# Performance work log

Measured on AMD Instinct MI355X. Metric: run time of the kernel, lower is better.

## Reference

```python
import jax, jax.numpy as jnp
import numpy as np

EPS = 1e-13

def masked_softmax(x, mask):
    # Non-memory-efficient path of the original: softmax(x*mask), re-mask, renormalize.
    p = jax.nn.softmax(x * mask, axis=-1) * mask
    return p / (jnp.sum(p, axis=-1, keepdims=True) + EPS)

def setup_inputs() -> dict:
    key = jax.random.key(0)
    ka, kb, kma, kmb = jax.random.split(key, 4)
    B, La, Lb, D = 32, 1024, 1024, 256
    a = jax.random.normal(ka, (B, La, D), dtype=jnp.float32)
    b = jax.random.normal(kb, (B, Lb, D), dtype=jnp.float32)
    mask_a = jax.random.randint(kma, (B, La, 1), 0, 2, dtype=jnp.int32)
    mask_b = jax.random.randint(kmb, (B, Lb, 1), 0, 2, dtype=jnp.int32)
    return {"a": a, "b": b, "mask_a": mask_a, "mask_b": mask_b}

def reference(a, b, mask_a, mask_b):
    # a: [B, La, D], b: [B, Lb, D], mask_a: [B, La, 1], mask_b: [B, Lb, 1]
    ma = mask_a.astype(a.dtype)  # [B, La, 1]
    mb = mask_b.astype(b.dtype)  # [B, Lb, 1]
    attn = jnp.einsum('bid,bjd->bij', a, b)            # [B, La, Lb]
    amask = ma * jnp.swapaxes(mb, 1, 2)                 # outer product mask [B, La, Lb]
    weight_for_a = masked_softmax(attn, amask)          # softmax over Lb
    attended_a = jnp.einsum('bij,bjd->bid', weight_for_a, b)  # [B, La, D]
    attn_t = jnp.swapaxes(attn, 1, 2)                   # [B, Lb, La]
    amask_t = jnp.swapaxes(amask, 1, 2)
    weight_for_b = masked_softmax(attn_t, amask_t)      # softmax over La
    attended_b = jnp.einsum('bji,bid->bjd', weight_for_b, a)  # [B, Lb, D]
    return (attended_a, attended_b)
```

## Files before the change

### kernel.cpp

```cpp
#include <hip/hip_runtime.h>
#include <math.h>
#include <stdint.h>


#define NB    32
#define SEQ   1024
#define DIM   256
#define BM    128
#define BN    64
#define SHIFT 60.0f
#define PS    1048

typedef unsigned int uint;
typedef unsigned short ushort;
typedef __attribute__((ext_vector_type(8)))  short short8;
typedef __attribute__((ext_vector_type(16))) float f32x16;

#define HL_BATCH  (64 * 1024 * 8)
#define HL_TENSOR ((size_t)NB * HL_BATCH)
#define T_BATCH   (128 * 256 * 8)
#define T_TENSOR  ((size_t)NB * T_BATCH)
#define WS_NEED   ((2 * HL_TENSOR + 2 * T_TENSOR) * sizeof(ushort))

__device__ __forceinline__ ushort bf16_rn(float x) {
    union { float f; uint u; } v; v.f = x;
    uint r = v.u + 0x7fffu + ((v.u >> 16) & 1u);
    return (ushort)(r >> 16);
}
__device__ __forceinline__ float bf16_to_f(ushort h) {
    union { uint u; float f; } v; v.u = ((uint)h) << 16;
    return v.f;
}
__device__ __forceinline__ void gl_lds16(const ushort* g, ushort* l) {
    __builtin_amdgcn_global_load_lds(
        (const __attribute__((address_space(1))) void*)g,
        (__attribute__((address_space(3))) void*)l, 16, 0, 0);
}

#define TSTR 264
__global__ __launch_bounds__(256)
void prepass(const float* __restrict__ A, const float* __restrict__ Bt,
             ushort* __restrict__ aHL, ushort* __restrict__ bHL,
             ushort* __restrict__ aT,  ushort* __restrict__ bT)
{
    const int tensor = blockIdx.z;
    const float* src = tensor ? Bt : A;
    ushort* hl = tensor ? bHL : aHL;
    ushort* tp = tensor ? bT  : aT;
    const int batch = blockIdx.y;
    const int tid   = threadIdx.x;

    __shared__ float tile[8 * TSTR];

    ushort* hlb = hl + (size_t)batch * HL_BATCH;

    for (int it = 0; it < 8; ++it) {
        const int soct = blockIdx.x * 8 + it;
        const int s0   = soct * 8;
        if (it) __syncthreads();

        {
            const int oct = tid >> 3, srow = tid & 7;
            const float* rp = src + ((size_t)batch * SEQ + s0 + srow) * DIM + oct * 8;
            float4 x0 = *(const float4*)rp;
            float4 x1 = *(const float4*)(rp + 4);
            float xs[8] = {x0.x, x0.y, x0.z, x0.w, x1.x, x1.y, x1.z, x1.w};
            short8 hv, lv;
            #pragma unroll
            for (int j = 0; j < 8; ++j) {
                ushort h = bf16_rn(xs[j]);
                hv[j] = (short)h;
                lv[j] = (short)bf16_rn(xs[j] - bf16_to_f(h));
            }
            *(short8*)(hlb + (size_t)oct * 8192 + (size_t)(s0 + srow) * 8)        = hv;
            *(short8*)(hlb + (size_t)(oct + 32) * 8192 + (size_t)(s0 + srow) * 8) = lv;
        }

        const float* sb = src + ((size_t)batch * SEQ + s0) * DIM;
        #pragma unroll
        for (int i = 0; i < 2; ++i) {
            int idx = tid + i * 256;
            int r = idx >> 6, c = idx & 63;
            float4 v = *((const float4*)(sb + (size_t)r * DIM) + c);
            *(float4*)&tile[r * TSTR + c * 4] = v;
        }
        __syncthreads();
        {
            ushort* tpb = tp + (size_t)batch * T_BATCH + (size_t)soct * 2048;
            int d = tid;
            short8 hv;
            #pragma unroll
            for (int j = 0; j < 8; ++j)
                hv[j] = (short)bf16_rn(tile[j * TSTR + d]);
            *(short8*)(tpb + (size_t)d * 8) = hv;
        }
    }
}

__global__ __launch_bounds__(512, 2)
void attend3(const ushort* __restrict__ aHL, const ushort* __restrict__ bHL,
             const ushort* __restrict__ aT,  const ushort* __restrict__ bT,
             const int*    __restrict__ ma,  const int*    __restrict__ mb,
             float*        __restrict__ out)
{
    __shared__ __align__(16) ushort Ks2[64 * 512];
    __shared__ __align__(16) ushort Vt2[8 * 2048];
    __shared__ __align__(16) ushort Ph[8 * PS];
    __shared__ float msk[SEQ];
    __shared__ float lpart[2][BM];
    __shared__ float invs[BM];

    const int bx   = blockIdx.x;
    const int xcd  = bx & 7;
    const int slot = bx >> 3;
    const int rb   = slot & 7;
    const int pg   = slot >> 3;
    const int pair = xcd + 8 * pg;
    const int batch = pair >> 1;
    const int dir   = pair & 1;
    const int row0  = rb * BM;

    const ushort* hlX = dir ? bHL : aHL;
    const ushort* hlY = dir ? aHL : bHL;
    const ushort* tY  = dir ? aT  : bT;
    const int*    mx  = dir ? mb  : ma;
    const int*    my  = dir ? ma  : mb;
    float* o = out + (size_t)dir * NB * SEQ * DIM;

    const int tid  = threadIdx.x;
    const int lane = tid & 63;
    const int wave = tid >> 6;
    const int l31  = lane & 31;
    const int lh   = lane >> 5;
    const int rw   = wave >> 1;
    const int cw   = wave & 1;

    const ushort* hlXb = hlX + (size_t)batch * HL_BATCH;
    const ushort* hlYb = hlY + (size_t)batch * HL_BATCH;
    const ushort* tYb  = tY  + (size_t)batch * T_BATCH;

    const ushort* ksrc = hlYb + (size_t)(wave * 8) * 8192 + (size_t)lane * 8;
    ushort*       kdst = Ks2 + wave * 8 * 512 + lane * 8;
    const ushort* vsrc = tYb + (size_t)wave * 2048 + (size_t)lane * 8;
    ushort*       vdst = Vt2 + wave * 2048 + lane * 8;

    #pragma unroll
    for (int i = 0; i < 8; ++i) gl_lds16(ksrc + (size_t)i * 8192, kdst + i * 512);
    #pragma unroll
    for (int i = 0; i < 4; ++i) gl_lds16(vsrc + i * 512, vdst + i * 512);

    for (int i = tid; i < SEQ; i += 512) msk[i] = (float)my[batch * SEQ + i];

    const int qrow = row0 + rw * 32 + l31;
    short8 qhi[16], qlo[16];
    {
        const ushort* qb = hlXb + (size_t)lh * 8192 + (size_t)qrow * 8;
        #pragma unroll
        for (int kk = 0; kk < 16; ++kk) {
            qhi[kk] = *(const short8*)(qb + (size_t)(2 * kk) * 8192);
            qlo[kk] = *(const short8*)(qb + (size_t)(2 * kk + 32) * 8192);
        }
    }

    f32x16 oacc[4];
    #pragma unroll
    for (int t = 0; t < 4; ++t)
        #pragma unroll
        for (int r = 0; r < 16; ++r) oacc[t][r] = 0.f;
    float lsum[16];
    #pragma unroll
    for (int r = 0; r < 16; ++r) lsum[r] = 0.f;

    __syncthreads();

    for (int nt = 0; nt < SEQ / BN; ++nt) {
        const int key0 = nt * BN;
        const float mkv = msk[key0 + cw * 32 + l31];

        f32x16 a1, a2;
        #pragma unroll
        for (int r = 0; r < 16; ++r) { a1[r] = 0.f; a2[r] = 0.f; }
        const int kcol = (cw * 32 + l31) * 8;
        #pragma unroll
        for (int kk = 0; kk < 16; ++kk) {
            short8 bhi = *(const short8*)&Ks2[(2 * kk + lh) * 512 + kcol];
            a1 = __builtin_amdgcn_mfma_f32_32x32x16_bf16(qhi[kk], bhi, a1, 0, 0, 0);
            a2 = __builtin_amdgcn_mfma_f32_32x32x16_bf16(qlo[kk], bhi, a2, 0, 0, 0);
        }
        #pragma unroll
        for (int kk = 0; kk < 16; ++kk) {
            short8 blo = *(const short8*)&Ks2[(2 * kk + lh + 32) * 512 + kcol];
            a2 = __builtin_amdgcn_mfma_f32_32x32x16_bf16(qhi[kk], blo, a2, 0, 0, 0);
        }

        const int key  = cw * 32 + l31;
        const int koct = key >> 3, kj = key & 7;
        #pragma unroll
        for (int r = 0; r < 16; ++r) {
            float s = a1[r] + a2[r];
            float p = __expf(s - SHIFT) * mkv;
            lsum[r] += p;
            int qr = rw * 32 + (r & 3) + ((r >> 2) << 3) + (lh << 2);
            Ph[koct * PS + qr * 8 + kj] = bf16_rn(p);
        }
        __syncthreads();

        if (nt + 1 < SEQ / BN) {
            const ushort* ks = ksrc + (size_t)(key0 + BN) * 8;
            #pragma unroll
            for (int i = 0; i < 8; ++i) gl_lds16(ks + (size_t)i * 8192, kdst + i * 512);
        }

        const int prow = (rw * 32 + l31) * 8;
        #pragma unroll
        for (int kb = 0; kb < 4; ++kb) {
            short8 pa = *(const short8*)&Ph[(2 * kb + lh) * PS + prow];
            #pragma unroll
            for (int t = 0; t < 4; ++t) {
                int dim = cw * 128 + t * 32 + l31;
                short8 vf = *(const short8*)&Vt2[(2 * kb + lh) * 2048 + dim * 8];
                oacc[t] = __builtin_amdgcn_mfma_f32_32x32x16_bf16(pa, vf, oacc[t], 0, 0, 0);
            }
        }
        __syncthreads();

        if (nt + 1 < SEQ / BN) {
            const ushort* vs = vsrc + ((size_t)(key0 + BN) >> 3) * 2048;
            #pragma unroll
            for (int i = 0; i < 4; ++i) gl_lds16(vs + i * 512, vdst + i * 512);
        }
    }

    #pragma unroll
    for (int r = 0; r < 16; ++r) {
        float v = lsum[r];
        v += __shfl_xor(v, 1, 64);
        v += __shfl_xor(v, 2, 64);
        v += __shfl_xor(v, 4, 64);
        v += __shfl_xor(v, 8, 64);
        v += __shfl_xor(v, 16, 64);
        if (l31 == 0) {
            int row = rw * 32 + (r & 3) + ((r >> 2) << 3) + (lh << 2);
            lpart[cw][row] = v;
        }
    }
    __syncthreads();
    if (tid < BM) {
        float l = lpart[0][tid] + lpart[1][tid];
        int valid = mx[batch * SEQ + row0 + tid];
        invs[tid] = (valid != 0 && l > 0.f) ? 1.f / l : 0.f;
    }
    __syncthreads();

    float* ob = o + ((size_t)batch * SEQ + row0) * DIM;
    #pragma unroll
    for (int r = 0; r < 16; ++r) {
        int rloc = rw * 32 + (r & 3) + ((r >> 2) << 3) + (lh << 2);
        float inv = invs[rloc];
        #pragma unroll
        for (int t = 0; t < 4; ++t) {
            int d = cw * 128 + t * 32 + l31;
            ob[(size_t)rloc * DIM + d] = oacc[t][r] * inv;
        }
    }
}

#define F_KS_STR 520
#define F_P_STR  136
#define F_BM 64
#define F_BN 64
__global__ __launch_bounds__(256, 1)
void attend_mfma(const float* __restrict__ X, const float* __restrict__ Y,
                 const int* __restrict__ mx, const int* __restrict__ my,
                 float* __restrict__ out)
{
    __shared__ ushort Ks[F_BN * F_KS_STR];
    __shared__ ushort Ps[F_BM * F_P_STR];
    __shared__ float  mk[F_BN];
    __shared__ float  lpart[2][F_BM];
    __shared__ float  invs[F_BM];

    const int tid = threadIdx.x, lane = tid & 63, wave = tid >> 6;
    const int l31 = lane & 31, lh = lane >> 5;
    const int rw = wave >> 1, cw = wave & 1;
    const int batch = blockIdx.y, row0 = blockIdx.x * F_BM;
    const float* Xb = X + (size_t)batch * SEQ * DIM;
    const float* Yb = Y + (size_t)batch * SEQ * DIM;

    float4 kreg[16]; int mreg = 0;
    #pragma unroll
    for (int i = 0; i < 16; ++i) {
        int idx = tid + (i << 8); int r = idx >> 6, c4 = idx & 63;
        kreg[i] = *((const float4*)(Yb + (size_t)r * DIM) + c4);
    }
    if (tid < F_BN) mreg = my[batch * SEQ + tid];

    short8 qhi[16], qlo[16];
    {
        const float* qrow = Xb + (size_t)(row0 + rw * 32 + l31) * DIM + lh * 8;
        #pragma unroll
        for (int kk = 0; kk < 16; ++kk) {
            const float* p = qrow + kk * 16;
            float4 x0 = *(const float4*)p; float4 x1 = *(const float4*)(p + 4);
            float xs[8] = {x0.x, x0.y, x0.z, x0.w, x1.x, x1.y, x1.z, x1.w};
            #pragma unroll
            for (int j = 0; j < 8; ++j) {
                ushort h = bf16_rn(xs[j]);
                qhi[kk][j] = (short)h;
                qlo[kk][j] = (short)bf16_rn(xs[j] - bf16_to_f(h));
            }
        }
    }
    f32x16 oacc[4];
    #pragma unroll
    for (int t = 0; t < 4; ++t)
        #pragma unroll
        for (int r = 0; r < 16; ++r) oacc[t][r] = 0.f;
    float lsum[16];
    #pragma unroll
    for (int r = 0; r < 16; ++r) lsum[r] = 0.f;

    for (int nt = 0; nt < SEQ / F_BN; ++nt) {
        if (nt) __syncthreads();
        #pragma unroll
        for (int i = 0; i < 16; ++i) {
            int idx = tid + (i << 8); int r = idx >> 6, c4 = idx & 63;
            float f[4] = {kreg[i].x, kreg[i].y, kreg[i].z, kreg[i].w};
            ushort hh[4], ll[4];
            #pragma unroll
            for (int q = 0; q < 4; ++q) { hh[q] = bf16_rn(f[q]); ll[q] = bf16_rn(f[q] - bf16_to_f(hh[q])); }
            ushort4 hv; hv.x=hh[0];hv.y=hh[1];hv.z=hh[2];hv.w=hh[3];
            ushort4 lv; lv.x=ll[0];lv.y=ll[1];lv.z=ll[2];lv.w=ll[3];
            *(ushort4*)&Ks[r * F_KS_STR + c4 * 4] = hv;
            *(ushort4*)&Ks[r * F_KS_STR + 256 + c4 * 4] = lv;
        }
        if (tid < F_BN) mk[tid] = (float)mreg;
        __syncthreads();
        if (nt + 1 < SEQ / F_BN) {
            const float* Ybn = Yb + (size_t)(nt + 1) * F_BN * DIM;
            #pragma unroll
            for (int i = 0; i < 16; ++i) {
                int idx = tid + (i << 8); int r = idx >> 6, c4 = idx & 63;
                kreg[i] = *((const float4*)(Ybn + (size_t)r * DIM) + c4);
            }
            if (tid < F_BN) mreg = my[batch * SEQ + (nt + 1) * F_BN + tid];
        }
        f32x16 a1, a2, a3;
        #pragma unroll
        for (int r = 0; r < 16; ++r) { a1[r]=0.f; a2[r]=0.f; a3[r]=0.f; }
        const int krow = (cw * 32 + l31) * F_KS_STR;
        #pragma unroll
        for (int kk = 0; kk < 16; ++kk) {
            int col = kk * 16 + lh * 8;
            short8 bhi = *(const short8*)&Ks[krow + col];
            short8 blo = *(const short8*)&Ks[krow + 256 + col];
            a1 = __builtin_amdgcn_mfma_f32_32x32x16_bf16(qhi[kk], bhi, a1, 0, 0, 0);
            a2 = __builtin_amdgcn_mfma_f32_32x32x16_bf16(qlo[kk], bhi, a2, 0, 0, 0);
            a3 = __builtin_amdgcn_mfma_f32_32x32x16_bf16(qhi[kk], blo, a3, 0, 0, 0);
        }
        const float mkv = mk[cw * 32 + l31];
        #pragma unroll
        for (int r = 0; r < 16; ++r) {
            float s = a1[r] + a2[r] + a3[r];
            float p = __expf(s - SHIFT) * mkv;
            lsum[r] += p;
            ushort ph = bf16_rn(p);
            ushort pl = bf16_rn(p - bf16_to_f(ph));
            int prow = rw * 32 + (r & 3) + ((r >> 2) << 3) + (lh << 2);
            int pcol = cw * 32 + l31;
            Ps[prow * F_P_STR + pcol] = ph;
            Ps[prow * F_P_STR + 64 + pcol] = pl;
        }
        __syncthreads();
        const int prow = (rw * 32 + l31) * F_P_STR;
        #pragma unroll
        for (int kb = 0; kb < 4; ++kb) {
            int pcol = kb * 16 + lh * 8;
            short8 pa_hi = *(const short8*)&Ps[prow + pcol];
            short8 pa_lo = *(const short8*)&Ps[prow + 64 + pcol];
            #pragma unroll
            for (int t = 0; t < 4; ++t) {
                int d0 = cw * 128 + t * 32 + l31;
                short8 vf;
                #pragma unroll
                for (int j = 0; j < 8; ++j) vf[j] = (short)Ks[(pcol + j) * F_KS_STR + d0];
                oacc[t] = __builtin_amdgcn_mfma_f32_32x32x16_bf16(pa_hi, vf, oacc[t], 0, 0, 0);
                oacc[t] = __builtin_amdgcn_mfma_f32_32x32x16_bf16(pa_lo, vf, oacc[t], 0, 0, 0);
            }
        }
    }
    #pragma unroll
    for (int r = 0; r < 16; ++r) {
        float v = lsum[r];
        v += __shfl_xor(v, 1, 64); v += __shfl_xor(v, 2, 64); v += __shfl_xor(v, 4, 64);
        v += __shfl_xor(v, 8, 64); v += __shfl_xor(v, 16, 64);
        if (l31 == 0) {
            int row = rw * 32 + (r & 3) + ((r >> 2) << 3) + (lh << 2);
            lpart[cw][row] = v;
        }
    }
    __syncthreads();
    if (tid < F_BM) {
        float l = lpart[0][tid] + lpart[1][tid];
        int valid = mx[batch * SEQ + row0 + tid];
        invs[tid] = (valid != 0 && l > 0.f) ? 1.f / l : 0.f;
    }
    __syncthreads();
    float* ob = out + ((size_t)batch * SEQ + row0) * DIM;
    #pragma unroll
    for (int r = 0; r < 16; ++r) {
        int rloc = rw * 32 + (r & 3) + ((r >> 2) << 3) + (lh << 2);
        float inv = invs[rloc];
        #pragma unroll
        for (int t = 0; t < 4; ++t) {
            int d = cw * 128 + t * 32 + l31;
            ob[(size_t)rloc * DIM + d] = oacc[t][r] * inv;
        }
    }
}

extern "C" void kernel_launch(void* const* d_in, const int* in_sizes, int n_in,
                              void* d_out, int out_size, void* d_ws, size_t ws_size,
                              hipStream_t stream) {
    const float* a  = (const float*)d_in[0];
    const float* b  = (const float*)d_in[1];
    const int*   ma = (const int*)d_in[2];
    const int*   mb = (const int*)d_in[3];
    float* out = (float*)d_out;

    if (ws_size >= WS_NEED) {
        ushort* wsu = (ushort*)d_ws;
        ushort* aHL = wsu;
        ushort* bHL = wsu + HL_TENSOR;
        ushort* aT  = wsu + 2 * HL_TENSOR;
        ushort* bT  = wsu + 2 * HL_TENSOR + T_TENSOR;

        prepass<<<dim3(SEQ / 64, NB, 2), 256, 0, stream>>>(a, b, aHL, bHL, aT, bT);
        attend3<<<dim3(512, 1, 1), 512, 0, stream>>>(aHL, bHL, aT, bT, ma, mb, out);
    } else {
        float* out_a = out;
        float* out_b = out + (size_t)NB * SEQ * DIM;
        dim3 grid(SEQ / F_BM, NB), block(256);
        attend_mfma<<<grid, block, 0, stream>>>(a, b, ma, mb, out_a);
        attend_mfma<<<grid, block, 0, stream>>>(b, a, mb, ma, out_b);
    }
}
```

Baseline: 317.2 us.

## Read V fragments directly from global, split accumulators, raise MFMA priority, widen prepass grid

The attention kernel stops staging V tiles into LDS and reads the transposed bf16 V fragments straight from global memory inside the PV MFMA loop. This drops the Vt2 buffer and its async copies and frees LDS. The QK cross-term now uses a third accumulator to break the dependency chain on a2, and s_setprio brackets the MFMA loops. The prepass is flattened to one 8-row octet per block with an 8x larger grid. The direct global V reads may expose latency that the LDS staging used to hide.

```diff
diff --git a/kernel.cpp b/kernel.cpp
--- a/kernel.cpp
+++ b/kernel.cpp
@@ -54,46 +54,43 @@
 
     ushort* hlb = hl + (size_t)batch * HL_BATCH;
 
-    for (int it = 0; it < 8; ++it) {
-        const int soct = blockIdx.x * 8 + it;
-        const int s0   = soct * 8;
-        if (it) __syncthreads();
-
-        {
-            const int oct = tid >> 3, srow = tid & 7;
-            const float* rp = src + ((size_t)batch * SEQ + s0 + srow) * DIM + oct * 8;
-            float4 x0 = *(const float4*)rp;
-            float4 x1 = *(const float4*)(rp + 4);
-            float xs[8] = {x0.x, x0.y, x0.z, x0.w, x1.x, x1.y, x1.z, x1.w};
-            short8 hv, lv;
-            #pragma unroll
-            for (int j = 0; j < 8; ++j) {
-                ushort h = bf16_rn(xs[j]);
-                hv[j] = (short)h;
-                lv[j] = (short)bf16_rn(xs[j] - bf16_to_f(h));
-            }
-            *(short8*)(hlb + (size_t)oct * 8192 + (size_t)(s0 + srow) * 8)        = hv;
-            *(short8*)(hlb + (size_t)(oct + 32) * 8192 + (size_t)(s0 + srow) * 8) = lv;
-        }
-
-        const float* sb = src + ((size_t)batch * SEQ + s0) * DIM;
-        #pragma unroll
-        for (int i = 0; i < 2; ++i) {
-            int idx = tid + i * 256;
-            int r = idx >> 6, c = idx & 63;
-            float4 v = *((const float4*)(sb + (size_t)r * DIM) + c);
-            *(float4*)&tile[r * TSTR + c * 4] = v;
-        }
-        __syncthreads();
-        {
-            ushort* tpb = tp + (size_t)batch * T_BATCH + (size_t)soct * 2048;
-            int d = tid;
-            short8 hv;
-            #pragma unroll
-            for (int j = 0; j < 8; ++j)
-                hv[j] = (short)bf16_rn(tile[j * TSTR + d]);
-            *(short8*)(tpb + (size_t)d * 8) = hv;
-        }
+    const int soct = blockIdx.x;
+    const int s0   = soct * 8;
+
+    {
+        const int oct = tid >> 3, srow = tid & 7;
+        const float* rp = src + ((size_t)batch * SEQ + s0 + srow) * DIM + oct * 8;
+        float4 x0 = *(const float4*)rp;
+        float4 x1 = *(const float4*)(rp + 4);
+        float xs[8] = {x0.x, x0.y, x0.z, x0.w, x1.x, x1.y, x1.z, x1.w};
+        short8 hv, lv;
+        #pragma unroll
+        for (int j = 0; j < 8; ++j) {
+            ushort h = bf16_rn(xs[j]);
+            hv[j] = (short)h;
+            lv[j] = (short)bf16_rn(xs[j] - bf16_to_f(h));
+        }
+        *(short8*)(hlb + (size_t)oct * 8192 + (size_t)(s0 + srow) * 8)        = hv;
+        *(short8*)(hlb + (size_t)(oct + 32) * 8192 + (size_t)(s0 + srow) * 8) = lv;
+    }
+
+    const float* sb = src + ((size_t)batch * SEQ + s0) * DIM;
+    #pragma unroll
+    for (int i = 0; i < 2; ++i) {
+        int idx = tid + i * 256;
+        int r = idx >> 6, c = idx & 63;
+        float4 v = *((const float4*)(sb + (size_t)r * DIM) + c);
+        *(float4*)&tile[r * TSTR + c * 4] = v;
+    }
+    __syncthreads();
+    {
+        ushort* tpb = tp + (size_t)batch * T_BATCH + (size_t)soct * 2048;
+        int d = tid;
+        short8 hv;
+        #pragma unroll
+        for (int j = 0; j < 8; ++j)
+            hv[j] = (short)bf16_rn(tile[j * TSTR + d]);
+        *(short8*)(tpb + (size_t)d * 8) = hv;
     }
 }
 
@@ -104,7 +101,6 @@
              float*        __restrict__ out)
 {
     __shared__ __align__(16) ushort Ks2[64 * 512];
-    __shared__ __align__(16) ushort Vt2[8 * 2048];
     __shared__ __align__(16) ushort Ph[8 * PS];
     __shared__ float msk[SEQ];
     __shared__ float lpart[2][BM];
@@ -141,13 +137,9 @@
 
     const ushort* ksrc = hlYb + (size_t)(wave * 8) * 8192 + (size_t)lane * 8;
     ushort*       kdst = Ks2 + wave * 8 * 512 + lane * 8;
-    const ushort* vsrc = tYb + (size_t)wave * 2048 + (size_t)lane * 8;
-    ushort*       vdst = Vt2 + wave * 2048 + lane * 8;
 
     #pragma unroll
     for (int i = 0; i < 8; ++i) gl_lds16(ksrc + (size_t)i * 8192, kdst + i * 512);
-    #pragma unroll
-    for (int i = 0; i < 4; ++i) gl_lds16(vsrc + i * 512, vdst + i * 512);
 
     for (int i = tid; i < SEQ; i += 512) msk[i] = (float)my[batch * SEQ + i];
 
@@ -177,10 +169,11 @@
         const int key0 = nt * BN;
         const float mkv = msk[key0 + cw * 32 + l31];
 
-        f32x16 a1, a2;
-        #pragma unroll
-        for (int r = 0; r < 16; ++r) { a1[r] = 0.f; a2[r] = 0.f; }
+        f32x16 a1, a2, a3;
+        #pragma unroll
+        for (int r = 0; r < 16; ++r) { a1[r] = 0.f; a2[r] = 0.f; a3[r] = 0.f; }
         const int kcol = (cw * 32 + l31) * 8;
+        __builtin_amdgcn_s_setprio(1);
         #pragma unroll
         for (int kk = 0; kk < 16; ++kk) {
             short8 bhi = *(const short8*)&Ks2[(2 * kk + lh) * 512 + kcol];
@@ -190,14 +183,15 @@
         #pragma unroll
         for (int kk = 0; kk < 16; ++kk) {
             short8 blo = *(const short8*)&Ks2[(2 * kk + lh + 32) * 512 + kcol];
-            a2 = __builtin_amdgcn_mfma_f32_32x32x16_bf16(qhi[kk], blo, a2, 0, 0, 0);
-        }
+            a3 = __builtin_amdgcn_mfma_f32_32x32x16_bf16(qhi[kk], blo, a3, 0, 0, 0);
+        }
+        __builtin_amdgcn_s_setprio(0);
 
         const int key  = cw * 32 + l31;
         const int koct = key >> 3, kj = key & 7;
         #pragma unroll
         for (int r = 0; r < 16; ++r) {
-            float s = a1[r] + a2[r];
+            float s = a1[r] + a2[r] + a3[r];
             float p = __expf(s - SHIFT) * mkv;
             lsum[r] += p;
             int qr = rw * 32 + (r & 3) + ((r >> 2) << 3) + (lh << 2);
@@ -212,23 +206,20 @@
         }
 
         const int prow = (rw * 32 + l31) * 8;
+        const ushort* vb = tYb + (size_t)(key0 >> 3) * 2048;
+        __builtin_amdgcn_s_setprio(1);
         #pragma unroll
         for (int kb = 0; kb < 4; ++kb) {
             short8 pa = *(const short8*)&Ph[(2 * kb + lh) * PS + prow];
             #pragma unroll
             for (int t = 0; t < 4; ++t) {
                 int dim = cw * 128 + t * 32 + l31;
-                short8 vf = *(const short8*)&Vt2[(2 * kb + lh) * 2048 + dim * 8];
+                short8 vf = *(const short8*)(vb + (size_t)(2 * kb + lh) * 2048 + (size_t)dim * 8);
                 oacc[t] = __builtin_amdgcn_mfma_f32_32x32x16_bf16(pa, vf, oacc[t], 0, 0, 0);
             }
         }
+        __builtin_amdgcn_s_setprio(0);
         __syncthreads();
-
-        if (nt + 1 < SEQ / BN) {
-            const ushort* vs = vsrc + ((size_t)(key0 + BN) >> 3) * 2048;
-            #pragma unroll
-            for (int i = 0; i < 4; ++i) gl_lds16(vs + i * 512, vdst + i * 512);
-        }
     }
 
     #pragma unroll
@@ -435,7 +426,7 @@
         ushort* aT  = wsu + 2 * HL_TENSOR;
         ushort* bT  = wsu + 2 * HL_TENSOR + T_TENSOR;
 
-        prepass<<<dim3(SEQ / 64, NB, 2), 256, 0, stream>>>(a, b, aHL, bHL, aT, bT);
+        prepass<<<dim3(SEQ / 8, NB, 2), 256, 0, stream>>>(a, b, aHL, bHL, aT, bT);
         attend3<<<dim3(512, 1, 1), 512, 0, stream>>>(aHL, bHL, aT, bT, ma, mb, out);
     } else {
         float* out_a = out;
```

Measured after the change: 399.7 us. +26.0%, slower.

## Compact valid keys per batch and skip fully masked key tiles

Applied to the files above, without the earlier changes.

Adds a compaction kernel that builds, per batch and tensor, a list of the indices of unmasked positions and their count. The attention kernel now gathers only those keys, both the split-bf16 K rows and a transposed V built by a new gather kernel, and loops only over the tiles that hold valid keys, so roughly half the QK and PV MFMA work is dropped for random binary masks. The prepass no longer writes the transposed copy and runs one octet per block. In exchange there are two extra kernel launches and gathered, index-driven K loads instead of contiguous streams.

```diff
diff --git a/kernel.cpp b/kernel.cpp
--- a/kernel.cpp
+++ b/kernel.cpp
@@ -20,7 +20,8 @@
 #define HL_TENSOR ((size_t)NB * HL_BATCH)
 #define T_BATCH   (128 * 256 * 8)
 #define T_TENSOR  ((size_t)NB * T_BATCH)
-#define WS_NEED   ((2 * HL_TENSOR + 2 * T_TENSOR) * sizeof(ushort))
+#define IDX_INTS  ((size_t)NB * SEQ)
+#define WS_NEED   ((2 * HL_TENSOR + 2 * T_TENSOR) * sizeof(ushort) + (2 * IDX_INTS + 64) * sizeof(int))
 
 __device__ __forceinline__ ushort bf16_rn(float x) {
     union { float f; uint u; } v; v.f = x;
@@ -37,76 +38,103 @@
         (__attribute__((address_space(3))) void*)l, 16, 0, 0);
 }
 
-#define TSTR 264
+__global__ __launch_bounds__(1024)
+void compact(const int* __restrict__ ma, const int* __restrict__ mb,
+             int* __restrict__ idxA, int* __restrict__ idxB, int* __restrict__ nvArr)
+{
+    const int batch = blockIdx.x;
+    const int t     = blockIdx.y;
+    const int* m = t ? mb : ma;
+    int* idx = (t ? idxB : idxA) + batch * SEQ;
+    const int tid = threadIdx.x;
+    const int lane = tid & 63, wv = tid >> 6;
+
+    __shared__ int wsum[16];
+    __shared__ int base[17];
+
+    int v = (m[batch * SEQ + tid] != 0) ? 1 : 0;
+    unsigned long long bal = __ballot(v);
+    int lanePre = __popcll(bal & ((1ULL << lane) - 1ULL));
+    if (lane == 0) wsum[wv] = __popcll(bal);
+    __syncthreads();
+    if (tid == 0) {
+        int acc = 0;
+        #pragma unroll
+        for (int w = 0; w < 16; ++w) { base[w] = acc; acc += wsum[w]; }
+        base[16] = acc;
+        nvArr[t * NB + batch] = acc;
+    }
+    __syncthreads();
+    if (v) idx[base[wv] + lanePre] = tid;
+    if (tid >= base[16]) idx[tid] = 0;
+}
+
 __global__ __launch_bounds__(256)
 void prepass(const float* __restrict__ A, const float* __restrict__ Bt,
-             ushort* __restrict__ aHL, ushort* __restrict__ bHL,
-             ushort* __restrict__ aT,  ushort* __restrict__ bT)
+             ushort* __restrict__ aHL, ushort* __restrict__ bHL)
 {
     const int tensor = blockIdx.z;
     const float* src = tensor ? Bt : A;
     ushort* hl = tensor ? bHL : aHL;
-    ushort* tp = tensor ? bT  : aT;
     const int batch = blockIdx.y;
     const int tid   = threadIdx.x;
 
-    __shared__ float tile[8 * TSTR];
-
     ushort* hlb = hl + (size_t)batch * HL_BATCH;
-
-    for (int it = 0; it < 8; ++it) {
-        const int soct = blockIdx.x * 8 + it;
-        const int s0   = soct * 8;
-        if (it) __syncthreads();
-
-        {
-            const int oct = tid >> 3, srow = tid & 7;
-            const float* rp = src + ((size_t)batch * SEQ + s0 + srow) * DIM + oct * 8;
-            float4 x0 = *(const float4*)rp;
-            float4 x1 = *(const float4*)(rp + 4);
-            float xs[8] = {x0.x, x0.y, x0.z, x0.w, x1.x, x1.y, x1.z, x1.w};
-            short8 hv, lv;
-            #pragma unroll
-            for (int j = 0; j < 8; ++j) {
-                ushort h = bf16_rn(xs[j]);
-                hv[j] = (short)h;
-                lv[j] = (short)bf16_rn(xs[j] - bf16_to_f(h));
-            }
-            *(short8*)(hlb + (size_t)oct * 8192 + (size_t)(s0 + srow) * 8)        = hv;
-            *(short8*)(hlb + (size_t)(oct + 32) * 8192 + (size_t)(s0 + srow) * 8) = lv;
-        }
-
-        const float* sb = src + ((size_t)batch * SEQ + s0) * DIM;
-        #pragma unroll
-        for (int i = 0; i < 2; ++i) {
-            int idx = tid + i * 256;
-            int r = idx >> 6, c = idx & 63;
-            float4 v = *((const float4*)(sb + (size_t)r * DIM) + c);
-            *(float4*)&tile[r * TSTR + c * 4] = v;
-        }
-        __syncthreads();
-        {
-            ushort* tpb = tp + (size_t)batch * T_BATCH + (size_t)soct * 2048;
-            int d = tid;
-            short8 hv;
-            #pragma unroll
-            for (int j = 0; j < 8; ++j)
-                hv[j] = (short)bf16_rn(tile[j * TSTR + d]);
-            *(short8*)(tpb + (size_t)d * 8) = hv;
-        }
-    }
+    const int soct = blockIdx.x;
+    const int s0   = soct * 8;
+    const int oct = tid >> 3, srow = tid & 7;
+    const float* rp = src + ((size_t)batch * SEQ + s0 + srow) * DIM + oct * 8;
+    float4 x0 = *(const float4*)rp;
+    float4 x1 = *(const float4*)(rp + 4);
+    float xs[8] = {x0.x, x0.y, x0.z, x0.w, x1.x, x1.y, x1.z, x1.w};
+    short8 hv, lv;
+    #pragma unroll
+    for (int j = 0; j < 8; ++j) {
+        ushort h = bf16_rn(xs[j]);
+        hv[j] = (short)h;
+        lv[j] = (short)bf16_rn(xs[j] - bf16_to_f(h));
+    }
+    *(short8*)(hlb + (size_t)oct * 8192 + (size_t)(s0 + srow) * 8)        = hv;
+    *(short8*)(hlb + (size_t)(oct + 32) * 8192 + (size_t)(s0 + srow) * 8) = lv;
+}
+
+__global__ __launch_bounds__(256)
+void gatherT(const float* __restrict__ A, const float* __restrict__ Bt,
+             const int* __restrict__ idxA, const int* __restrict__ idxB,
+             const int* __restrict__ nvArr,
+             ushort* __restrict__ aT, ushort* __restrict__ bT)
+{
+    const int z     = blockIdx.z;
+    const int batch = blockIdx.y;
+    const int soct  = blockIdx.x;
+    const float* src = z ? Bt : A;
+    const int* idx = (z ? idxB : idxA) + batch * SEQ;
+    const int nv = nvArr[z * NB + batch];
+    ushort* tp = (z ? bT : aT) + (size_t)batch * T_BATCH + (size_t)soct * 2048;
+    const int d = threadIdx.x;
+    short8 hv;
+    #pragma unroll
+    for (int j = 0; j < 8; ++j) {
+        int c = soct * 8 + j;
+        float x = 0.f;
+        if (c < nv) x = src[((size_t)batch * SEQ + idx[c]) * DIM + d];
+        hv[j] = (short)bf16_rn(x);
+    }
+    *(short8*)(tp + (size_t)d * 8) = hv;
 }
 
 __global__ __launch_bounds__(512, 2)
 void attend3(const ushort* __restrict__ aHL, const ushort* __restrict__ bHL,
              const ushort* __restrict__ aT,  const ushort* __restrict__ bT,
+             const int*    __restrict__ idxA, const int* __restrict__ idxB,
+             const int*    __restrict__ nvArr,
              const int*    __restrict__ ma,  const int*    __restrict__ mb,
              float*        __restrict__ out)
 {
     __shared__ __align__(16) ushort Ks2[64 * 512];
     __shared__ __align__(16) ushort Vt2[8 * 2048];
     __shared__ __align__(16) ushort Ph[8 * PS];
-    __shared__ float msk[SEQ];
+    __shared__ int   kidx[SEQ];
     __shared__ float lpart[2][BM];
     __shared__ float invs[BM];
 
@@ -124,7 +152,9 @@
     const ushort* hlY = dir ? aHL : bHL;
     const ushort* tY  = dir ? aT  : bT;
     const int*    mx  = dir ? mb  : ma;
-    const int*    my  = dir ? ma  : mb;
+    const int*    idxY = dir ? idxA : idxB;
+    const int     nv   = nvArr[(dir ? 0 : 1) * NB + batch];
+    const int     ntiles = (nv + BN - 1) >> 6;
     float* o = out + (size_t)dir * NB * SEQ * DIM;
 
     const int tid  = threadIdx.x;
@@ -139,17 +169,20 @@
     const ushort* hlYb = hlY + (size_t)batch * HL_BATCH;
     const ushort* tYb  = tY  + (size_t)batch * T_BATCH;
 
-    const ushort* ksrc = hlYb + (size_t)(wave * 8) * 8192 + (size_t)lane * 8;
+    for (int i = tid; i < SEQ; i += 512) kidx[i] = idxY[batch * SEQ + i];
+    __syncthreads();
+
     ushort*       kdst = Ks2 + wave * 8 * 512 + lane * 8;
     const ushort* vsrc = tYb + (size_t)wave * 2048 + (size_t)lane * 8;
     ushort*       vdst = Vt2 + wave * 2048 + lane * 8;
 
-    #pragma unroll
-    for (int i = 0; i < 8; ++i) gl_lds16(ksrc + (size_t)i * 8192, kdst + i * 512);
-    #pragma unroll
-    for (int i = 0; i < 4; ++i) gl_lds16(vsrc + i * 512, vdst + i * 512);
-
-    for (int i = tid; i < SEQ; i += 512) msk[i] = (float)my[batch * SEQ + i];
+    {
+        const ushort* ks = hlYb + (size_t)(wave * 8) * 8192 + (size_t)kidx[lane] * 8;
+        #pragma unroll
+        for (int i = 0; i < 8; ++i) gl_lds16(ks + (size_t)i * 8192, kdst + i * 512);
+        #pragma unroll
+        for (int i = 0; i < 4; ++i) gl_lds16(vsrc + i * 512, vdst + i * 512);
+    }
 
     const int qrow = row0 + rw * 32 + l31;
     short8 qhi[16], qlo[16];
@@ -173,9 +206,9 @@
 
     __syncthreads();
 
-    for (int nt = 0; nt < SEQ / BN; ++nt) {
+    for (int nt = 0; nt < ntiles; ++nt) {
         const int key0 = nt * BN;
-        const float mkv = msk[key0 + cw * 32 + l31];
+        const float mkv = (key0 + cw * 32 + l31 < nv) ? 1.f : 0.f;
 
         f32x16 a1, a2;
         #pragma unroll
@@ -205,8 +238,9 @@
         }
         __syncthreads();
 
-        if (nt + 1 < SEQ / BN) {
-            const ushort* ks = ksrc + (size_t)(key0 + BN) * 8;
+        if (nt + 1 < ntiles) {
+            const int kg = kidx[key0 + BN + lane];
+            const ushort* ks = hlYb + (size_t)(wave * 8) * 8192 + (size_t)kg * 8;
             #pragma unroll
             for (int i = 0; i < 8; ++i) gl_lds16(ks + (size_t)i * 8192, kdst + i * 512);
         }
@@ -224,7 +258,7 @@
         }
         __syncthreads();
 
-        if (nt + 1 < SEQ / BN) {
+        if (nt + 1 < ntiles) {
             const ushort* vs = vsrc + ((size_t)(key0 + BN) >> 3) * 2048;
             #pragma unroll
             for (int i = 0; i < 4; ++i) gl_lds16(vs + i * 512, vdst + i * 512);
@@ -434,9 +468,15 @@
         ushort* bHL = wsu + HL_TENSOR;
         ushort* aT  = wsu + 2 * HL_TENSOR;
         ushort* bT  = wsu + 2 * HL_TENSOR + T_TENSOR;
-
-        prepass<<<dim3(SEQ / 64, NB, 2), 256, 0, stream>>>(a, b, aHL, bHL, aT, bT);
-        attend3<<<dim3(512, 1, 1), 512, 0, stream>>>(aHL, bHL, aT, bT, ma, mb, out);
+        int* idxA  = (int*)(wsu + 2 * HL_TENSOR + 2 * T_TENSOR);
+        int* idxB  = idxA + IDX_INTS;
+        int* nvArr = idxB + IDX_INTS;
+
+        compact<<<dim3(NB, 2), 1024, 0, stream>>>(ma, mb, idxA, idxB, nvArr);
+        prepass<<<dim3(SEQ / 8, NB, 2), 256, 0, stream>>>(a, b, aHL, bHL);
+        gatherT<<<dim3(128, NB, 2), 256, 0, stream>>>(a, b, idxA, idxB, nvArr, aT, bT);
+        attend3<<<dim3(512, 1, 1), 512, 0, stream>>>(aHL, bHL, aT, bT,
+                                                     idxA, idxB, nvArr, ma, mb, out);
     } else {
         float* out_a = out;
         float* out_b = out + (size_t)NB * SEQ * DIM;
```

Result: faster. 307.3 us (-3.1%).
